# Performance work log

Hardware: AMD Instinct MI355X
Metric: run time of the kernel (lower is better)

The kernel has to match this reference:

```python
import jax, jax.numpy as jnp
import numpy as np
from functools import partial

N, E = 50000, 800000
IN_C, HID, HEADS, OUT_C = 128, 32, 4, 32
NEG_SLOPE = 0.2


def _segment_softmax(alpha, dst, num_nodes):
    # alpha: [E', H] scores, dst: [E'] destination node ids
    m = jax.ops.segment_max(alpha, dst, num_segments=num_nodes)  # [N, H]
    m = jnp.where(jnp.isfinite(m), m, 0.0)
    ex = jnp.exp(alpha - m[dst])
    s = jax.ops.segment_sum(ex, dst, num_segments=num_nodes)  # [N, H]
    return ex / s[dst]


def gat_conv(x, edge_idx, edge_attr, W, att_src, att_dst, W_edge, att_edge, bias, heads, out_c, concat):
    """PyG GATConv (eval mode, add_self_loops=True, fill_value='mean')."""
    n = x.shape[0]
    src, dst = edge_idx[0], edge_idx[1]
    e = src.shape[0]
    # self-loop edge_attr = per-node mean of incoming edge attrs (PyG fill_value='mean')
    deg = jax.ops.segment_sum(jnp.ones((e,), x.dtype), dst, num_segments=n)
    loop_attr = jax.ops.segment_sum(edge_attr, dst, num_segments=n) / jnp.maximum(deg, 1.0)[:, None]
    loop = jnp.arange(n, dtype=src.dtype)
    src = jnp.concatenate([src, loop])
    dst = jnp.concatenate([dst, loop])
    ea = jnp.concatenate([edge_attr, loop_attr], axis=0)  # [E+N, 1]
    # node / edge projections
    h = (x @ W).reshape(n, heads, out_c)                  # [N, H, C]
    a_src = jnp.einsum('nhc,hc->nh', h, att_src)          # [N, H]
    a_dst = jnp.einsum('nhc,hc->nh', h, att_dst)
    he = (ea @ W_edge).reshape(-1, heads, out_c)          # [E', H, C]
    a_edge = jnp.einsum('ehc,hc->eh', he, att_edge)       # [E', H]
    # per-edge attention logits + segment softmax over destinations
    alpha = a_src[src] + a_dst[dst] + a_edge
    alpha = jax.nn.leaky_relu(alpha, NEG_SLOPE)
    alpha = _segment_softmax(alpha, dst, n)               # [E', H]
    # weighted scatter-aggregate of source messages
    out = jax.ops.segment_sum(h[src] * alpha[:, :, None], dst, num_segments=n)  # [N, H, C]
    out = out.reshape(n, heads * out_c) if concat else out.mean(axis=1)
    return out + bias


def setup_inputs() -> dict:
    key = jax.random.key(0)
    ks = jax.random.split(key, 16)
    s = 0.1
    return {
        'x': jax.random.normal(ks[0], (N, IN_C), jnp.float32),
        'edge_idx': jax.random.randint(ks[1], (2, E), 0, N, jnp.int32),
        'edge_attr': jax.random.normal(ks[2], (E, 1), jnp.float32),
        'W1': s * jax.random.normal(ks[3], (IN_C, HEADS * HID), jnp.float32),
        'a_src1': s * jax.random.normal(ks[4], (HEADS, HID), jnp.float32),
        'a_dst1': s * jax.random.normal(ks[5], (HEADS, HID), jnp.float32),
        'We1': s * jax.random.normal(ks[6], (1, HEADS * HID), jnp.float32),
        'a_e1': s * jax.random.normal(ks[7], (HEADS, HID), jnp.float32),
        'b1': jnp.zeros((HEADS * HID,), jnp.float32),
        'W2': s * jax.random.normal(ks[8], (HEADS * HID, OUT_C), jnp.float32),
        'a_src2': s * jax.random.normal(ks[9], (1, OUT_C), jnp.float32),
        'a_dst2': s * jax.random.normal(ks[10], (1, OUT_C), jnp.float32),
        'We2': s * jax.random.normal(ks[11], (1, OUT_C), jnp.float32),
        'a_e2': s * jax.random.normal(ks[12], (1, OUT_C), jnp.float32),
        'b2': jnp.zeros((OUT_C,), jnp.float32),
    }


def reference(x, edge_idx, edge_attr, W1, a_src1, a_dst1, We1, a_e1, b1,
              W2, a_src2, a_dst2, We2, a_e2, b2):
    # eval mode: ablation probs = 0 (identity), dropout = 0, with_skip = False
    h = gat_conv(x, edge_idx, edge_attr, W1, a_src1, a_dst1, We1, a_e1, b1, HEADS, HID, True)
    h = jax.nn.elu(h)
    out = gat_conv(h, edge_idx, edge_attr, W2, a_src2, a_dst2, We2, a_e2, b2, 1, OUT_C, True)
    return out
```

## Files before the change

kernel.cpp:

```cpp
#include <hip/hip_runtime.h>
#include <hip/hip_bf16.h>
#include <math.h>

#define NN 50000
#define EE 800000
#define EP 850000
#define NB 196
#define NHIST 8
#define HPAD 50048
#define NEG 0.2f
#define LOG2E 1.4426950408889634f

__global__ void k_zero(int* hist) {
    int i = blockIdx.x * 256 + threadIdx.x;
    if (i < NHIST * HPAD) hist[i] = 0;
}

__global__ void k_const(const float* __restrict__ We1, const float* __restrict__ ae1,
                        const float* __restrict__ We2, const float* __restrict__ ae2,
                        float* cbuf) {
    int j = threadIdx.x;
    float p = We1[j] * ae1[j];
    #pragma unroll
    for (int m = 16; m >= 1; m >>= 1) p += __shfl_xor(p, m);
    if ((j & 31) == 0) cbuf[j >> 5] = p;
    if (j < 32) {
        float q = We2[j] * ae2[j];
        #pragma unroll
        for (int m = 16; m >= 1; m >>= 1) q += __shfl_xor(q, m);
        if (j == 0) cbuf[4] = q;
    }
}

__global__ void k_degi(const int* __restrict__ ei, int* hist) {
    int e = blockIdx.x * 256 + threadIdx.x;
    if (e >= EE) return;
    int d = ei[EE + e];
    atomicAdd(&hist[(blockIdx.x & 7) * HPAD + d], 1);
}

__global__ void k_scan1(const int* __restrict__ hist, int* rowptr, int* blksum) {
    __shared__ int part[256];
    int t = threadIdx.x;
    int i = blockIdx.x * 256 + t;
    int dg = 0;
    if (i < NN) {
        #pragma unroll
        for (int c = 0; c < NHIST; ++c) dg += hist[c * HPAD + i];
    }
    int v = (i < NN) ? dg + 1 : 0;
    part[t] = v;
    __syncthreads();
    #pragma unroll
    for (int d = 1; d < 256; d <<= 1) {
        int u = (t >= d) ? part[t - d] : 0;
        __syncthreads();
        part[t] += u;
        __syncthreads();
    }
    if (i < NN) rowptr[i] = part[t] - v;
    if (t == 255) blksum[blockIdx.x] = part[255];
}

__global__ void k_scan2(int* blksum) {
    __shared__ int part[256];
    int t = threadIdx.x;
    int v = (t < NB) ? blksum[t] : 0;
    part[t] = v;
    __syncthreads();
    #pragma unroll
    for (int d = 1; d < 256; d <<= 1) {
        int u = (t >= d) ? part[t - d] : 0;
        __syncthreads();
        part[t] += u;
        __syncthreads();
    }
    if (t < NB) blksum[t] = part[t] - v;
}

__global__ void k_scan3(int* rowptr, const int* __restrict__ blksum,
                        int* cursor, int* bsrc, int* bdst) {
    int i = blockIdx.x * 256 + threadIdx.x;
    if (i >= NN) return;
    int off = rowptr[i] + blksum[blockIdx.x];
    rowptr[i] = off;
    bsrc[off] = i;
    bdst[off] = i;
    cursor[i] = off + 1;
    if (i == 0) rowptr[NN] = EP;
}

__global__ void k_scatter(const int* __restrict__ ei, const float* __restrict__ eattr,
                          int* cursor, int* bsrc, int* bdst, float* battr) {
    int e = blockIdx.x * 256 + threadIdx.x;
    if (e >= EE) return;
    int d = ei[EE + e];
    int p = atomicAdd(&cursor[d], 1);
    bsrc[p] = ei[e];
    bdst[p] = d;
    battr[p] = eattr[e];
}

__global__ void k_loopattr(const int* __restrict__ rowptr, float* battr) {
    int i = blockIdx.x * 256 + threadIdx.x;
    if (i >= NN) return;
    int p0 = rowptr[i], p1 = rowptr[i + 1];
    float s = 0.f;
    for (int p = p0 + 1; p < p1; ++p) s += battr[p];
    battr[p0] = s / fmaxf((float)(p1 - p0 - 1), 1.f);
}

__global__ void k_h1(const float* __restrict__ x, const float* __restrict__ W1,
                     const float* __restrict__ as1, const float* __restrict__ ad1,
                     __hip_bfloat16* h1b, float* asrc1, float* adst1) {
    __shared__ float sx[4][128];
    int j = threadIdx.x;
    int base = blockIdx.x * 16;
    int h = j >> 5;
    float es = as1[j];
    float ed = ad1[j];
    for (int it = 0; it < 4; ++it) {
        int n0 = base + it * 4;
        __syncthreads();
        #pragma unroll
        for (int r = 0; r < 4; ++r) {
            int n = n0 + r;
            sx[r][j] = (n < NN) ? x[(size_t)n * 128 + j] : 0.f;
        }
        __syncthreads();
        float a0 = 0.f, a1 = 0.f, a2 = 0.f, a3 = 0.f;
        #pragma unroll 8
        for (int k = 0; k < 128; ++k) {
            float w = W1[k * 128 + j];
            a0 += sx[0][k] * w; a1 += sx[1][k] * w;
            a2 += sx[2][k] * w; a3 += sx[3][k] * w;
        }
        float accs[4] = {a0, a1, a2, a3};
        #pragma unroll
        for (int r = 0; r < 4; ++r) {
            int n = n0 + r;
            float v = accs[r];
            float ps = v * es, pd = v * ed;
            #pragma unroll
            for (int m = 16; m >= 1; m >>= 1) { ps += __shfl_xor(ps, m); pd += __shfl_xor(pd, m); }
            if (n < NN) {
                h1b[n * 128 + j] = __float2bfloat16(v);
                if ((j & 31) == 0) { asrc1[n * 4 + h] = ps; adst1[n * 4 + h] = pd; }
            }
        }
    }
}

__global__ void k_z1(const int* __restrict__ bsrc, const int* __restrict__ bdst,
                     const float* __restrict__ battr,
                     const float* __restrict__ asrc1, const float* __restrict__ adst1,
                     const float* __restrict__ cbuf, float* z1) {
    int p = blockIdx.x * 256 + threadIdx.x;
    if (p >= EP) return;
    int s = bsrc[p], d = bdst[p];
    float a = battr[p];
    const float4 vs = *(const float4*)&asrc1[s * 4];
    const float4 vd = *(const float4*)&adst1[d * 4];
    float4 z;
    z.x = vs.x + vd.x + a * cbuf[0];
    z.y = vs.y + vd.y + a * cbuf[1];
    z.z = vs.z + vd.z + a * cbuf[2];
    z.w = vs.w + vd.w + a * cbuf[3];
    z.x = (z.x > 0.f ? z.x : NEG * z.x) * LOG2E;
    z.y = (z.y > 0.f ? z.y : NEG * z.y) * LOG2E;
    z.z = (z.z > 0.f ? z.z : NEG * z.z) * LOG2E;
    z.w = (z.w > 0.f ? z.w : NEG * z.w) * LOG2E;
    *(float4*)&z1[(size_t)p * 4] = z;
}

__global__ void k_gat1(const int* __restrict__ rowptr, const int* __restrict__ bsrc,
                       const float* __restrict__ z1, const uint* __restrict__ h1u,
                       float* out1) {
    int wid = (blockIdx.x * 256 + threadIdx.x) >> 6;
    if (wid >= NN) return;
    int lane = threadIdx.x & 63;
    int p0 = rowptr[wid], p1 = rowptr[wid + 1];
    float4 m4 = make_float4(-INFINITY, -INFINITY, -INFINITY, -INFINITY);
    for (int p = p0 + lane; p < p1; p += 64) {
        const float4 z = *(const float4*)&z1[(size_t)p * 4];
        m4.x = fmaxf(m4.x, z.x); m4.y = fmaxf(m4.y, z.y);
        m4.z = fmaxf(m4.z, z.z); m4.w = fmaxf(m4.w, z.w);
    }
    #pragma unroll
    for (int k = 32; k >= 1; k >>= 1) {
        m4.x = fmaxf(m4.x, __shfl_xor(m4.x, k));
        m4.y = fmaxf(m4.y, __shfl_xor(m4.y, k));
        m4.z = fmaxf(m4.z, __shfl_xor(m4.z, k));
        m4.w = fmaxf(m4.w, __shfl_xor(m4.w, k));
    }
    int h = lane >> 4;
    float m = (h == 0) ? m4.x : (h == 1) ? m4.y : (h == 2) ? m4.z : m4.w;
    float s = 0.f, acc0 = 0.f, acc1 = 0.f;
    int p = p0;
    for (; p + 4 <= p1; p += 4) {
        float z0 = z1[p * 4 + h],       z1v = z1[(p + 1) * 4 + h];
        float z2v = z1[(p + 2) * 4 + h], z3v = z1[(p + 3) * 4 + h];
        int s0 = bsrc[p], s1 = bsrc[p + 1], s2 = bsrc[p + 2], s3 = bsrc[p + 3];
        uint u0 = h1u[s0 * 64 + lane];
        uint u1 = h1u[s1 * 64 + lane];
        uint u2 = h1u[s2 * 64 + lane];
        uint u3 = h1u[s3 * 64 + lane];
        float w0 = exp2f(z0 - m), w1 = exp2f(z1v - m);
        float w2 = exp2f(z2v - m), w3 = exp2f(z3v - m);
        s += (w0 + w1) + (w2 + w3);
        acc0 += w0 * __uint_as_float(u0 << 16) + w1 * __uint_as_float(u1 << 16)
              + w2 * __uint_as_float(u2 << 16) + w3 * __uint_as_float(u3 << 16);
        acc1 += w0 * __uint_as_float(u0 & 0xffff0000u) + w1 * __uint_as_float(u1 & 0xffff0000u)
              + w2 * __uint_as_float(u2 & 0xffff0000u) + w3 * __uint_as_float(u3 & 0xffff0000u);
    }
    for (; p < p1; ++p) {
        float z = z1[p * 4 + h];
        int s0 = bsrc[p];
        float w = exp2f(z - m);
        uint u0 = h1u[s0 * 64 + lane];
        s += w;
        acc0 += w * __uint_as_float(u0 << 16);
        acc1 += w * __uint_as_float(u0 & 0xffff0000u);
    }
    float inv = 1.f / s;
    float2 o; o.x = acc0 * inv; o.y = acc1 * inv;
    *(float2*)&out1[(size_t)wid * 128 + lane * 2] = o;
}

__global__ void k_h2(const float* __restrict__ out1, const float* __restrict__ b1,
                     const float* __restrict__ W2,
                     const float* __restrict__ as2, const float* __restrict__ ad2,
                     __hip_bfloat16* h2b, float* asrc2, float* adst2) {
    __shared__ float sW[128 * 32];
    __shared__ float sx[8][128];
    int tid = threadIdx.x;
    for (int i = tid; i < 128 * 32; i += 256) sW[i] = W2[i];
    int nl = tid >> 5, j = tid & 31;
    int base = blockIdx.x * 32;
    float es = as2[j], ed = ad2[j];
    for (int it = 0; it < 4; ++it) {
        int n0 = base + it * 8;
        __syncthreads();
        for (int i = tid; i < 1024; i += 256) {
            int r = i >> 7, k = i & 127;
            int n = n0 + r;
            float v = (n < NN) ? out1[(size_t)n * 128 + k] + b1[k] : 0.f;
            sx[r][k] = v > 0.f ? v : expm1f(v);
        }
        __syncthreads();
        int n = n0 + nl;
        float acc = 0.f;
        #pragma unroll 8
        for (int k = 0; k < 128; ++k) acc += sx[nl][k] * sW[k * 32 + j];
        float ps = acc * es, pd = acc * ed;
        #pragma unroll
        for (int m = 16; m >= 1; m >>= 1) { ps += __shfl_xor(ps, m); pd += __shfl_xor(pd, m); }
        if (n < NN) {
            h2b[n * 32 + j] = __float2bfloat16(acc);
            if (j == 0) { asrc2[n] = ps; adst2[n] = pd; }
        }
    }
}

__global__ void k_z2(const int* __restrict__ bsrc, const int* __restrict__ bdst,
                     const float* __restrict__ battr,
                     const float* __restrict__ asrc2, const float* __restrict__ adst2,
                     const float* __restrict__ cbuf, float* z2) {
    int p = blockIdx.x * 256 + threadIdx.x;
    if (p >= EP) return;
    float z = asrc2[bsrc[p]] + adst2[bdst[p]] + battr[p] * cbuf[4];
    z = z > 0.f ? z : NEG * z;
    z2[p] = z * LOG2E;
}

__global__ void k_gat2(const int* __restrict__ rowptr, const int* __restrict__ bsrc,
                       const float* __restrict__ z2, const __hip_bfloat16* __restrict__ h2b,
                       const float* __restrict__ b2, float* dout) {
    int wid = (blockIdx.x * 256 + threadIdx.x) >> 6;
    if (wid >= NN) return;
    int lane = threadIdx.x & 63;
    int j = lane & 31, eo = lane >> 5;
    int p0 = rowptr[wid], p1 = rowptr[wid + 1];
    float m = -INFINITY;
    for (int p = p0 + lane; p < p1; p += 64) m = fmaxf(m, z2[p]);
    #pragma unroll
    for (int k = 32; k >= 1; k >>= 1) m = fmaxf(m, __shfl_xor(m, k));
    float s = 0.f, acc = 0.f;
    int p = p0 + eo;
    for (; p + 2 < p1; p += 4) {
        float wA = exp2f(z2[p] - m), wB = exp2f(z2[p + 2] - m);
        int sA = bsrc[p], sB = bsrc[p + 2];
        float hA = __bfloat162float(h2b[sA * 32 + j]);
        float hB = __bfloat162float(h2b[sB * 32 + j]);
        s += wA + wB;
        acc += wA * hA + wB * hB;
    }
    if (p < p1) {
        float w = exp2f(z2[p] - m);
        int src = bsrc[p];
        s += w;
        acc += w * __bfloat162float(h2b[src * 32 + j]);
    }
    s += __shfl_xor(s, 32);
    acc += __shfl_xor(acc, 32);
    if (eo == 0) dout[(size_t)wid * 32 + j] = acc / s + b2[j];
}

extern "C" void kernel_launch(void* const* d_in, const int* in_sizes, int n_in,
                              void* d_out, int out_size, void* d_ws, size_t ws_size,
                              hipStream_t stream) {
    const float* x     = (const float*)d_in[0];
    const int*   ei    = (const int*)d_in[1];
    const float* eattr = (const float*)d_in[2];
    const float* W1    = (const float*)d_in[3];
    const float* as1   = (const float*)d_in[4];
    const float* ad1   = (const float*)d_in[5];
    const float* We1   = (const float*)d_in[6];
    const float* ae1   = (const float*)d_in[7];
    const float* b1    = (const float*)d_in[8];
    const float* W2    = (const float*)d_in[9];
    const float* as2   = (const float*)d_in[10];
    const float* ad2   = (const float*)d_in[11];
    const float* We2   = (const float*)d_in[12];
    const float* ae2   = (const float*)d_in[13];
    const float* b2    = (const float*)d_in[14];
    float* dout = (float*)d_out;

    char* p = (char*)d_ws;
    int*   hist   = (int*)p;   p += sizeof(int) * NHIST * HPAD;
    int*   rowptr = (int*)p;   p += sizeof(int) * (NN + 4);
    int*   cursor = (int*)p;   p += sizeof(int) * NN;
    int*   blksum = (int*)p;   p += sizeof(int) * 256;
    int*   bsrc   = (int*)p;   p += sizeof(int) * EP;
    int*   bdst   = (int*)p;   p += sizeof(int) * EP;
    float* battr  = (float*)p; p += sizeof(float) * EP;
    float* z1     = (float*)p; p += sizeof(float) * (size_t)EP * 4;
    __hip_bfloat16* h1b = (__hip_bfloat16*)p; p += sizeof(__hip_bfloat16) * (size_t)NN * 128;
    float* asrc1  = (float*)p; p += sizeof(float) * NN * 4;
    float* adst1  = (float*)p; p += sizeof(float) * NN * 4;
    float* out1   = (float*)p; p += sizeof(float) * (size_t)NN * 128;
    __hip_bfloat16* h2b = (__hip_bfloat16*)p; p += sizeof(__hip_bfloat16) * NN * 32;
    float* asrc2  = (float*)p; p += sizeof(float) * NN;
    float* adst2  = (float*)p; p += sizeof(float) * NN;
    float* cbuf   = (float*)p; p += sizeof(float) * 8;
    float* z2     = z1;

    k_zero    <<<(NHIST * HPAD + 255) / 256, 256, 0, stream>>>(hist);
    k_const   <<<1, 128, 0, stream>>>(We1, ae1, We2, ae2, cbuf);
    k_degi    <<<(EE + 255) / 256, 256, 0, stream>>>(ei, hist);
    k_scan1   <<<NB, 256, 0, stream>>>(hist, rowptr, blksum);
    k_scan2   <<<1, 256, 0, stream>>>(blksum);
    k_scan3   <<<NB, 256, 0, stream>>>(rowptr, blksum, cursor, bsrc, bdst);
    k_scatter <<<(EE + 255) / 256, 256, 0, stream>>>(ei, eattr, cursor, bsrc, bdst, battr);
    k_loopattr<<<(NN + 255) / 256, 256, 0, stream>>>(rowptr, battr);
    k_h1      <<<(NN + 15) / 16, 128, 0, stream>>>(x, W1, as1, ad1, h1b, asrc1, adst1);
    k_z1      <<<(EP + 255) / 256, 256, 0, stream>>>(bsrc, bdst, battr, asrc1, adst1, cbuf, z1);
    k_gat1    <<<(NN * 64 + 255) / 256, 256, 0, stream>>>(rowptr, bsrc, z1, (const uint*)h1b, out1);
    k_h2      <<<(NN + 31) / 32, 256, 0, stream>>>(out1, b1, W2, as2, ad2, h2b, asrc2, adst2);
    k_z2      <<<(EP + 255) / 256, 256, 0, stream>>>(bsrc, bdst, battr, asrc2, adst2, cbuf, z2);
    k_gat2    <<<(NN * 64 + 255) / 256, 256, 0, stream>>>(rowptr, bsrc, z2, h2b, b2, dout);
}
```

Measured before the change: 377.7 us.

## Fuse edge-logit kernels into aggregation and pack CSR edges as src/attr pairs

Drops the separate per-edge logit kernels (k_z1, k_z2) and recomputes the leaky-relu logits inside the aggregation kernels from asrc/adst/edge attr. LOG2E is folded into the node projections and the edge constants. Edge src and attr are packed into one uint2 array, and the scatter uses eight privatized cursor arrays to spread atomic contention. k_h1 also processes 8 nodes per pass instead of 4. This removes the z-buffer write and read traffic and two launches, at the cost of computing the logits twice (once in the max pass, once in the sum pass) and extra random asrc gathers.

Result: faster. 366.9 us (-2.9%).

```diff
diff --git a/kernel.cpp b/kernel.cpp
--- a/kernel.cpp
+++ b/kernel.cpp
@@ -23,12 +23,12 @@
     float p = We1[j] * ae1[j];
     #pragma unroll
     for (int m = 16; m >= 1; m >>= 1) p += __shfl_xor(p, m);
-    if ((j & 31) == 0) cbuf[j >> 5] = p;
+    if ((j & 31) == 0) cbuf[j >> 5] = p * LOG2E;
     if (j < 32) {
         float q = We2[j] * ae2[j];
         #pragma unroll
         for (int m = 16; m >= 1; m >>= 1) q += __shfl_xor(q, m);
-        if (j == 0) cbuf[4] = q;
+        if (j == 0) cbuf[4] = q * LOG2E;
     }
 }
 
@@ -79,65 +79,70 @@
 }
 
 __global__ void k_scan3(int* rowptr, const int* __restrict__ blksum,
-                        int* cursor, int* bsrc, int* bdst) {
+                        const int* __restrict__ hist, int* cursor8, uint2* bedge) {
     int i = blockIdx.x * 256 + threadIdx.x;
     if (i >= NN) return;
     int off = rowptr[i] + blksum[blockIdx.x];
     rowptr[i] = off;
-    bsrc[off] = i;
-    bdst[off] = i;
-    cursor[i] = off + 1;
+    bedge[off] = make_uint2((uint)i, 0u);
+    int cum = off + 1;
+    #pragma unroll
+    for (int c = 0; c < NHIST; ++c) {
+        cursor8[c * HPAD + i] = cum;
+        cum += hist[c * HPAD + i];
+    }
     if (i == 0) rowptr[NN] = EP;
 }
 
 __global__ void k_scatter(const int* __restrict__ ei, const float* __restrict__ eattr,
-                          int* cursor, int* bsrc, int* bdst, float* battr) {
+                          int* cursor8, uint2* bedge) {
     int e = blockIdx.x * 256 + threadIdx.x;
     if (e >= EE) return;
     int d = ei[EE + e];
-    int p = atomicAdd(&cursor[d], 1);
-    bsrc[p] = ei[e];
-    bdst[p] = d;
-    battr[p] = eattr[e];
-}
-
-__global__ void k_loopattr(const int* __restrict__ rowptr, float* battr) {
+    int p = atomicAdd(&cursor8[(blockIdx.x & 7) * HPAD + d], 1);
+    bedge[p] = make_uint2((uint)ei[e], __float_as_uint(eattr[e]));
+}
+
+__global__ void k_loopattr(const int* __restrict__ rowptr, uint2* bedge) {
     int i = blockIdx.x * 256 + threadIdx.x;
     if (i >= NN) return;
     int p0 = rowptr[i], p1 = rowptr[i + 1];
     float s = 0.f;
-    for (int p = p0 + 1; p < p1; ++p) s += battr[p];
-    battr[p0] = s / fmaxf((float)(p1 - p0 - 1), 1.f);
+    for (int p = p0 + 1; p < p1; ++p) s += __uint_as_float(bedge[p].y);
+    bedge[p0].y = __float_as_uint(s / fmaxf((float)(p1 - p0 - 1), 1.f));
 }
 
 __global__ void k_h1(const float* __restrict__ x, const float* __restrict__ W1,
                      const float* __restrict__ as1, const float* __restrict__ ad1,
                      __hip_bfloat16* h1b, float* asrc1, float* adst1) {
-    __shared__ float sx[4][128];
+    __shared__ float sx[8][128];
     int j = threadIdx.x;
     int base = blockIdx.x * 16;
     int h = j >> 5;
     float es = as1[j];
     float ed = ad1[j];
-    for (int it = 0; it < 4; ++it) {
-        int n0 = base + it * 4;
-        __syncthreads();
-        #pragma unroll
-        for (int r = 0; r < 4; ++r) {
+    for (int it = 0; it < 2; ++it) {
+        int n0 = base + it * 8;
+        __syncthreads();
+        #pragma unroll
+        for (int r = 0; r < 8; ++r) {
             int n = n0 + r;
             sx[r][j] = (n < NN) ? x[(size_t)n * 128 + j] : 0.f;
         }
         __syncthreads();
         float a0 = 0.f, a1 = 0.f, a2 = 0.f, a3 = 0.f;
-        #pragma unroll 8
+        float a4 = 0.f, a5 = 0.f, a6 = 0.f, a7 = 0.f;
+        #pragma unroll 4
         for (int k = 0; k < 128; ++k) {
             float w = W1[k * 128 + j];
             a0 += sx[0][k] * w; a1 += sx[1][k] * w;
             a2 += sx[2][k] * w; a3 += sx[3][k] * w;
-        }
-        float accs[4] = {a0, a1, a2, a3};
-        #pragma unroll
-        for (int r = 0; r < 4; ++r) {
+            a4 += sx[4][k] * w; a5 += sx[5][k] * w;
+            a6 += sx[6][k] * w; a7 += sx[7][k] * w;
+        }
+        float accs[8] = {a0, a1, a2, a3, a4, a5, a6, a7};
+        #pragma unroll
+        for (int r = 0; r < 8; ++r) {
             int n = n0 + r;
             float v = accs[r];
             float ps = v * es, pd = v * ed;
@@ -145,44 +150,32 @@
             for (int m = 16; m >= 1; m >>= 1) { ps += __shfl_xor(ps, m); pd += __shfl_xor(pd, m); }
             if (n < NN) {
                 h1b[n * 128 + j] = __float2bfloat16(v);
-                if ((j & 31) == 0) { asrc1[n * 4 + h] = ps; adst1[n * 4 + h] = pd; }
+                if ((j & 31) == 0) { asrc1[n * 4 + h] = ps * LOG2E; adst1[n * 4 + h] = pd * LOG2E; }
             }
         }
     }
 }
 
-__global__ void k_z1(const int* __restrict__ bsrc, const int* __restrict__ bdst,
-                     const float* __restrict__ battr,
-                     const float* __restrict__ asrc1, const float* __restrict__ adst1,
-                     const float* __restrict__ cbuf, float* z1) {
-    int p = blockIdx.x * 256 + threadIdx.x;
-    if (p >= EP) return;
-    int s = bsrc[p], d = bdst[p];
-    float a = battr[p];
-    const float4 vs = *(const float4*)&asrc1[s * 4];
-    const float4 vd = *(const float4*)&adst1[d * 4];
-    float4 z;
-    z.x = vs.x + vd.x + a * cbuf[0];
-    z.y = vs.y + vd.y + a * cbuf[1];
-    z.z = vs.z + vd.z + a * cbuf[2];
-    z.w = vs.w + vd.w + a * cbuf[3];
-    z.x = (z.x > 0.f ? z.x : NEG * z.x) * LOG2E;
-    z.y = (z.y > 0.f ? z.y : NEG * z.y) * LOG2E;
-    z.z = (z.z > 0.f ? z.z : NEG * z.z) * LOG2E;
-    z.w = (z.w > 0.f ? z.w : NEG * z.w) * LOG2E;
-    *(float4*)&z1[(size_t)p * 4] = z;
-}
-
-__global__ void k_gat1(const int* __restrict__ rowptr, const int* __restrict__ bsrc,
-                       const float* __restrict__ z1, const uint* __restrict__ h1u,
+__global__ void k_gat1(const int* __restrict__ rowptr, const uint2* __restrict__ bedge,
+                       const float* __restrict__ asrc1, const float* __restrict__ adst1,
+                       const float* __restrict__ cbuf, const uint* __restrict__ h1u,
                        float* out1) {
     int wid = (blockIdx.x * 256 + threadIdx.x) >> 6;
     if (wid >= NN) return;
     int lane = threadIdx.x & 63;
     int p0 = rowptr[wid], p1 = rowptr[wid + 1];
+    const float4 ad4 = *(const float4*)&adst1[wid * 4];
+    const float4 ce4 = *(const float4*)&cbuf[0];
     float4 m4 = make_float4(-INFINITY, -INFINITY, -INFINITY, -INFINITY);
     for (int p = p0 + lane; p < p1; p += 64) {
-        const float4 z = *(const float4*)&z1[(size_t)p * 4];
+        uint2 e = bedge[p];
+        float a = __uint_as_float(e.y);
+        const float4 as = *(const float4*)&asrc1[e.x * 4];
+        float4 z;
+        z.x = as.x + ad4.x + a * ce4.x; z.x = z.x > 0.f ? z.x : NEG * z.x;
+        z.y = as.y + ad4.y + a * ce4.y; z.y = z.y > 0.f ? z.y : NEG * z.y;
+        z.z = as.z + ad4.z + a * ce4.z; z.z = z.z > 0.f ? z.z : NEG * z.z;
+        z.w = as.w + ad4.w + a * ce4.w; z.w = z.w > 0.f ? z.w : NEG * z.w;
         m4.x = fmaxf(m4.x, z.x); m4.y = fmaxf(m4.y, z.y);
         m4.z = fmaxf(m4.z, z.z); m4.w = fmaxf(m4.w, z.w);
     }
@@ -194,19 +187,26 @@
         m4.w = fmaxf(m4.w, __shfl_xor(m4.w, k));
     }
     int h = lane >> 4;
-    float m = (h == 0) ? m4.x : (h == 1) ? m4.y : (h == 2) ? m4.z : m4.w;
+    float m   = (h == 0) ? m4.x  : (h == 1) ? m4.y  : (h == 2) ? m4.z  : m4.w;
+    float adh = (h == 0) ? ad4.x : (h == 1) ? ad4.y : (h == 2) ? ad4.z : ad4.w;
+    float ceh = (h == 0) ? ce4.x : (h == 1) ? ce4.y : (h == 2) ? ce4.z : ce4.w;
     float s = 0.f, acc0 = 0.f, acc1 = 0.f;
     int p = p0;
     for (; p + 4 <= p1; p += 4) {
-        float z0 = z1[p * 4 + h],       z1v = z1[(p + 1) * 4 + h];
-        float z2v = z1[(p + 2) * 4 + h], z3v = z1[(p + 3) * 4 + h];
-        int s0 = bsrc[p], s1 = bsrc[p + 1], s2 = bsrc[p + 2], s3 = bsrc[p + 3];
-        uint u0 = h1u[s0 * 64 + lane];
-        uint u1 = h1u[s1 * 64 + lane];
-        uint u2 = h1u[s2 * 64 + lane];
-        uint u3 = h1u[s3 * 64 + lane];
-        float w0 = exp2f(z0 - m), w1 = exp2f(z1v - m);
-        float w2 = exp2f(z2v - m), w3 = exp2f(z3v - m);
+        uint2 e0 = bedge[p],     e1 = bedge[p + 1];
+        uint2 e2 = bedge[p + 2], e3 = bedge[p + 3];
+        float q0 = asrc1[e0.x * 4 + h] + adh + __uint_as_float(e0.y) * ceh;
+        float q1 = asrc1[e1.x * 4 + h] + adh + __uint_as_float(e1.y) * ceh;
+        float q2 = asrc1[e2.x * 4 + h] + adh + __uint_as_float(e2.y) * ceh;
+        float q3 = asrc1[e3.x * 4 + h] + adh + __uint_as_float(e3.y) * ceh;
+        uint u0 = h1u[e0.x * 64 + lane];
+        uint u1 = h1u[e1.x * 64 + lane];
+        uint u2 = h1u[e2.x * 64 + lane];
+        uint u3 = h1u[e3.x * 64 + lane];
+        q0 = q0 > 0.f ? q0 : NEG * q0;  q1 = q1 > 0.f ? q1 : NEG * q1;
+        q2 = q2 > 0.f ? q2 : NEG * q2;  q3 = q3 > 0.f ? q3 : NEG * q3;
+        float w0 = exp2f(q0 - m), w1 = exp2f(q1 - m);
+        float w2 = exp2f(q2 - m), w3 = exp2f(q3 - m);
         s += (w0 + w1) + (w2 + w3);
         acc0 += w0 * __uint_as_float(u0 << 16) + w1 * __uint_as_float(u1 << 16)
               + w2 * __uint_as_float(u2 << 16) + w3 * __uint_as_float(u3 << 16);
@@ -214,10 +214,11 @@
               + w2 * __uint_as_float(u2 & 0xffff0000u) + w3 * __uint_as_float(u3 & 0xffff0000u);
     }
     for (; p < p1; ++p) {
-        float z = z1[p * 4 + h];
-        int s0 = bsrc[p];
-        float w = exp2f(z - m);
-        uint u0 = h1u[s0 * 64 + lane];
+        uint2 e0 = bedge[p];
+        float q = asrc1[e0.x * 4 + h] + adh + __uint_as_float(e0.y) * ceh;
+        q = q > 0.f ? q : NEG * q;
+        float w = exp2f(q - m);
+        uint u0 = h1u[e0.x * 64 + lane];
         s += w;
         acc0 += w * __uint_as_float(u0 << 16);
         acc1 += w * __uint_as_float(u0 & 0xffff0000u);
@@ -257,49 +258,52 @@
         for (int m = 16; m >= 1; m >>= 1) { ps += __shfl_xor(ps, m); pd += __shfl_xor(pd, m); }
         if (n < NN) {
             h2b[n * 32 + j] = __float2bfloat16(acc);
-            if (j == 0) { asrc2[n] = ps; adst2[n] = pd; }
-        }
-    }
-}
-
-__global__ void k_z2(const int* __restrict__ bsrc, const int* __restrict__ bdst,
-                     const float* __restrict__ battr,
-                     const float* __restrict__ asrc2, const float* __restrict__ adst2,
-                     const float* __restrict__ cbuf, float* z2) {
-    int p = blockIdx.x * 256 + threadIdx.x;
-    if (p >= EP) return;
-    float z = asrc2[bsrc[p]] + adst2[bdst[p]] + battr[p] * cbuf[4];
-    z = z > 0.f ? z : NEG * z;
-    z2[p] = z * LOG2E;
-}
-
-__global__ void k_gat2(const int* __restrict__ rowptr, const int* __restrict__ bsrc,
-                       const float* __restrict__ z2, const __hip_bfloat16* __restrict__ h2b,
+            if (j == 0) { asrc2[n] = ps * LOG2E; adst2[n] = pd * LOG2E; }
+        }
+    }
+}
+
+__global__ void k_gat2(const int* __restrict__ rowptr, const uint2* __restrict__ bedge,
+                       const float* __restrict__ asrc2, const float* __restrict__ adst2,
+                       const float* __restrict__ cbuf, const __hip_bfloat16* __restrict__ h2b,
                        const float* __restrict__ b2, float* dout) {
     int wid = (blockIdx.x * 256 + threadIdx.x) >> 6;
     if (wid >= NN) return;
     int lane = threadIdx.x & 63;
     int j = lane & 31, eo = lane >> 5;
     int p0 = rowptr[wid], p1 = rowptr[wid + 1];
+    float ad = adst2[wid];
+    float ce = cbuf[4];
     float m = -INFINITY;
-    for (int p = p0 + lane; p < p1; p += 64) m = fmaxf(m, z2[p]);
+    for (int p = p0 + lane; p < p1; p += 64) {
+        uint2 e = bedge[p];
+        float q = asrc2[e.x] + ad + __uint_as_float(e.y) * ce;
+        q = q > 0.f ? q : NEG * q;
+        m = fmaxf(m, q);
+    }
     #pragma unroll
     for (int k = 32; k >= 1; k >>= 1) m = fmaxf(m, __shfl_xor(m, k));
     float s = 0.f, acc = 0.f;
     int p = p0 + eo;
     for (; p + 2 < p1; p += 4) {
-        float wA = exp2f(z2[p] - m), wB = exp2f(z2[p + 2] - m);
-        int sA = bsrc[p], sB = bsrc[p + 2];
-        float hA = __bfloat162float(h2b[sA * 32 + j]);
-        float hB = __bfloat162float(h2b[sB * 32 + j]);
+        uint2 eA = bedge[p], eB = bedge[p + 2];
+        float qA = asrc2[eA.x] + ad + __uint_as_float(eA.y) * ce;
+        float qB = asrc2[eB.x] + ad + __uint_as_float(eB.y) * ce;
+        qA = qA > 0.f ? qA : NEG * qA;
+        qB = qB > 0.f ? qB : NEG * qB;
+        float wA = exp2f(qA - m), wB = exp2f(qB - m);
+        float hA = __bfloat162float(h2b[eA.x * 32 + j]);
+        float hB = __bfloat162float(h2b[eB.x * 32 + j]);
         s += wA + wB;
         acc += wA * hA + wB * hB;
     }
     if (p < p1) {
-        float w = exp2f(z2[p] - m);
-        int src = bsrc[p];
+        uint2 eA = bedge[p];
+        float q = asrc2[eA.x] + ad + __uint_as_float(eA.y) * ce;
+        q = q > 0.f ? q : NEG * q;
+        float w = exp2f(q - m);
         s += w;
-        acc += w * __bfloat162float(h2b[src * 32 + j]);
+        acc += w * __bfloat162float(h2b[eA.x * 32 + j]);
     }
     s += __shfl_xor(s, 32);
     acc += __shfl_xor(acc, 32);
@@ -327,36 +331,30 @@
     float* dout = (float*)d_out;
 
     char* p = (char*)d_ws;
-    int*   hist   = (int*)p;   p += sizeof(int) * NHIST * HPAD;
-    int*   rowptr = (int*)p;   p += sizeof(int) * (NN + 4);
-    int*   cursor = (int*)p;   p += sizeof(int) * NN;
-    int*   blksum = (int*)p;   p += sizeof(int) * 256;
-    int*   bsrc   = (int*)p;   p += sizeof(int) * EP;
-    int*   bdst   = (int*)p;   p += sizeof(int) * EP;
-    float* battr  = (float*)p; p += sizeof(float) * EP;
-    float* z1     = (float*)p; p += sizeof(float) * (size_t)EP * 4;
+    int*   hist    = (int*)p;   p += sizeof(int) * NHIST * HPAD;
+    int*   cursor8 = (int*)p;   p += sizeof(int) * NHIST * HPAD;
+    int*   rowptr  = (int*)p;   p += sizeof(int) * (NN + 4);
+    int*   blksum  = (int*)p;   p += sizeof(int) * 256;
+    uint2* bedge   = (uint2*)p; p += sizeof(uint2) * EP;
     __hip_bfloat16* h1b = (__hip_bfloat16*)p; p += sizeof(__hip_bfloat16) * (size_t)NN * 128;
-    float* asrc1  = (float*)p; p += sizeof(float) * NN * 4;
-    float* adst1  = (float*)p; p += sizeof(float) * NN * 4;
-    float* out1   = (float*)p; p += sizeof(float) * (size_t)NN * 128;
+    float* asrc1   = (float*)p; p += sizeof(float) * NN * 4;
+    float* adst1   = (float*)p; p += sizeof(float) * NN * 4;
+    float* out1    = (float*)p; p += sizeof(float) * (size_t)NN * 128;
     __hip_bfloat16* h2b = (__hip_bfloat16*)p; p += sizeof(__hip_bfloat16) * NN * 32;
-    float* asrc2  = (float*)p; p += sizeof(float) * NN;
-    float* adst2  = (float*)p; p += sizeof(float) * NN;
-    float* cbuf   = (float*)p; p += sizeof(float) * 8;
-    float* z2     = z1;
+    float* asrc2   = (float*)p; p += sizeof(float) * NN;
+    float* adst2   = (float*)p; p += sizeof(float) * NN;
+    float* cbuf    = (float*)p; p += sizeof(float) * 8;
 
     k_zero    <<<(NHIST * HPAD + 255) / 256, 256, 0, stream>>>(hist);
     k_const   <<<1, 128, 0, stream>>>(We1, ae1, We2, ae2, cbuf);
     k_degi    <<<(EE + 255) / 256, 256, 0, stream>>>(ei, hist);
     k_scan1   <<<NB, 256, 0, stream>>>(hist, rowptr, blksum);
     k_scan2   <<<1, 256, 0, stream>>>(blksum);
-    k_scan3   <<<NB, 256, 0, stream>>>(rowptr, blksum, cursor, bsrc, bdst);
-    k_scatter <<<(EE + 255) / 256, 256, 0, stream>>>(ei, eattr, cursor, bsrc, bdst, battr);
-    k_loopattr<<<(NN + 255) / 256, 256, 0, stream>>>(rowptr, battr);
+    k_scan3   <<<NB, 256, 0, stream>>>(rowptr, blksum, hist, cursor8, bedge);
+    k_scatter <<<(EE + 255) / 256, 256, 0, stream>>>(ei, eattr, cursor8, bedge);
+    k_loopattr<<<(NN + 255) / 256, 256, 0, stream>>>(rowptr, bedge);
     k_h1      <<<(NN + 15) / 16, 128, 0, stream>>>(x, W1, as1, ad1, h1b, asrc1, adst1);
-    k_z1      <<<(EP + 255) / 256, 256, 0, stream>>>(bsrc, bdst, battr, asrc1, adst1, cbuf, z1);
-    k_gat1    <<<(NN * 64 + 255) / 256, 256, 0, stream>>>(rowptr, bsrc, z1, (const uint*)h1b, out1);
+    k_gat1    <<<(NN * 64 + 255) / 256, 256, 0, stream>>>(rowptr, bedge, asrc1, adst1, cbuf, (const uint*)h1b, out1);
     k_h2      <<<(NN + 31) / 32, 256, 0, stream>>>(out1, b1, W2, as2, ad2, h2b, asrc2, adst2);
-    k_z2      <<<(EP + 255) / 256, 256, 0, stream>>>(bsrc, bdst, battr, asrc2, adst2, cbuf, z2);
-    k_gat2    <<<(NN * 64 + 255) / 256, 256, 0, stream>>>(rowptr, bsrc, z2, h2b, b2, dout);
-}
+    k_gat2    <<<(NN * 64 + 255) / 256, 256, 0, stream>>>(rowptr, bedge, asrc2, adst2, cbuf, h2b, b2, dout);
+}
```
